# Performance work log

Hardware: AMD Instinct MI355X
Metric: run time of the kernel (lower is better)

The kernel has to match this reference:

```python
import jax, jax.numpy as jnp
import numpy as np
import math

D_MODEL = 1024
EXPAND = 2
D_INNER = D_MODEL * EXPAND          # 2048
D_STATE = 16
NHEADS = 8
NGROUPS = 1
D_CONV = 4
HEADDIM = D_INNER // NHEADS         # 256
CONV_DIM = D_INNER + 2 * NGROUPS * D_STATE   # x, B, C go through the causal conv
D_IN_PROJ = 2 * D_INNER + 2 * NGROUPS * D_STATE + NHEADS  # z, xBC, dt
CHUNK = 64
BATCH = 4
SEQLEN = 4096


def setup_inputs() -> dict:
    key = jax.random.key(0)
    ks = jax.random.split(key, 6)
    rng = np.random.default_rng(0)
    u = jax.random.normal(ks[0], (BATCH, SEQLEN, D_MODEL), dtype=jnp.float32)
    W_in = jax.random.normal(ks[1], (D_MODEL, D_IN_PROJ), dtype=jnp.float32) * 0.02
    conv_w = jax.random.normal(ks[2], (CONV_DIM, D_CONV), dtype=jnp.float32) * (1.0 / math.sqrt(D_CONV))
    conv_b = jnp.zeros((CONV_DIM,), dtype=jnp.float32)
    # dt_bias = inverse-softplus of dt sampled log-uniform in [dt_min, dt_max]
    dt = np.exp(rng.uniform(size=NHEADS) * (math.log(0.1) - math.log(0.001)) + math.log(0.001))
    dt = np.clip(dt, 1e-4, None)
    dt_bias = jnp.asarray(dt + np.log(-np.expm1(-dt)), dtype=jnp.float32)
    # A in A_init_range=(0.9, 0.999), stored as A_log with A = -exp(A_log)
    A_log = jnp.asarray(np.log(rng.uniform(0.9, 0.999, NHEADS)), dtype=jnp.float32)
    D = jnp.ones((NHEADS,), dtype=jnp.float32)
    norm_w = jnp.ones((D_INNER,), dtype=jnp.float32)
    W_out = jax.random.normal(ks[3], (D_INNER, D_MODEL), dtype=jnp.float32) * 0.02
    return {"u": u, "W_in": W_in, "conv_w": conv_w, "conv_b": conv_b,
            "dt_bias": dt_bias, "A_log": A_log, "D": D, "norm_w": norm_w, "W_out": W_out}


def _mamba2_fwd(u, W_in, conv_w, conv_b, dt_bias, A_log, D, norm_w, W_out):
    b, l, _ = u.shape
    h, p, n, g, Q = NHEADS, HEADDIM, D_STATE, NGROUPS, CHUNK
    zxbcdt = u @ W_in                                   # [b,l,2*d_inner+2gn+h]
    z = zxbcdt[..., :D_INNER]
    xBC = zxbcdt[..., D_INNER:D_INNER + CONV_DIM]
    dt = jax.nn.softplus(zxbcdt[..., D_INNER + CONV_DIM:] + dt_bias)  # [b,l,h]
    # causal depthwise conv over time (d_conv taps) + SiLU
    xp = jnp.pad(xBC, ((0, 0), (D_CONV - 1, 0), (0, 0)))
    xconv = conv_b
    for k in range(D_CONV):
        xconv = xconv + xp[:, k:k + l, :] * conv_w[:, k]
    xBC = jax.nn.silu(xconv)
    x = xBC[..., :D_INNER].reshape(b, l, h, p)
    B = xBC[..., D_INNER:D_INNER + g * n].reshape(b, l, g, n)
    C = xBC[..., D_INNER + g * n:].reshape(b, l, g, n)
    Bh = jnp.repeat(B, h // g, axis=2)                  # [b,l,h,n]
    Ch = jnp.repeat(C, h // g, axis=2)
    A = -jnp.exp(A_log)                                 # [h]
    # ---- chunked (SSD) selective scan ----
    nc = l // Q
    xc = x.reshape(b, nc, Q, h, p)
    dtc = dt.reshape(b, nc, Q, h)
    Bc = Bh.reshape(b, nc, Q, h, n)
    Cc = Ch.reshape(b, nc, Q, h, n)
    a = dtc * A                                         # [b,nc,Q,h]
    cs = jnp.cumsum(a, axis=2).transpose(0, 1, 3, 2)    # [b,nc,h,Q]
    mask = jnp.tril(jnp.ones((Q, Q), dtype=bool))
    L = jnp.where(mask, jnp.exp(cs[..., :, None] - cs[..., None, :]), 0.0)  # [b,nc,h,Q,Q]
    xdt = xc * dtc[..., None]                           # x scaled by dt
    Y_diag = jnp.einsum('bcqhn,bcshn,bchqs,bcshp->bcqhp', Cc, Bc, L, xdt)
    decay_states = jnp.exp(cs[..., -1:] - cs)           # [b,nc,h,Q]
    states = jnp.einsum('bcqhn,bchq,bcqhp->bchpn', Bc, decay_states, xdt)  # per-chunk state
    chunk_decay = jnp.exp(cs[..., -1])                  # [b,nc,h]
    def step(carry, inp):
        st, dec = inp
        new = dec[..., None, None] * carry + st
        return new, carry
    init = jnp.zeros((b, h, p, n), dtype=u.dtype)
    _, prev = jax.lax.scan(step, init, (states.transpose(1, 0, 2, 3, 4), chunk_decay.transpose(1, 0, 2)))
    prev = prev.transpose(1, 0, 2, 3, 4)                # state entering each chunk [b,nc,h,p,n]
    Y_off = jnp.einsum('bcqhn,bchpn,bchq->bcqhp', Cc, prev, jnp.exp(cs))
    y = (Y_diag + Y_off).reshape(b, l, h, p) + D[:, None] * x
    y = y.reshape(b, l, D_INNER)
    # gated RMSNorm then out projection
    y = y * jax.nn.silu(z)
    y = y * jax.lax.rsqrt(jnp.mean(y * y, axis=-1, keepdims=True) + 1e-5) * norm_w
    return y @ W_out


def reference(u, W_in, conv_w, conv_b, dt_bias, A_log, D, norm_w, W_out):
    return _mamba2_fwd(u, W_in, conv_w, conv_b, dt_bias, A_log, D, norm_w, W_out)
```

## Files before the change

kernel.cpp:

```cpp
#include <hip/hip_runtime.h>
#include <cstddef>
#include <cstdint>

constexpr int DM = 1024;
constexpr int DI = 2048;
constexpr int DS = 16;
constexpr int NH = 8;
constexpr int CD = 2080;
constexpr int DP = 4136;
constexpr int DPT = 4352;
constexpr int Q  = 64;
constexpr int B_ = 4;
constexpr int L_ = 4096;
constexpr int NCH = 64;
constexpr int HP = 256;
constexpr int NR = B_ * L_;

constexpr size_t AL(size_t x) { return (x + 255) & ~(size_t)255; }
constexpr size_t OFFB_ZX = 0;
constexpr size_t OFFB_BC = AL(OFFB_ZX + (size_t)NR * DP * 2);
constexpr size_t OFFB_DT = AL(OFFB_BC + (size_t)NR * 32 * 4);
constexpr size_t OFFB_CS = AL(OFFB_DT + (size_t)NR * NH * 4);
constexpr size_t OFFB_ST = AL(OFFB_CS + (size_t)B_ * NCH * NH * Q * 4);
constexpr size_t OFFB_Y  = AL(OFFB_ST + (size_t)B_ * NCH * NH * HP * DS * 4);
constexpr size_t OFFB_WO = AL(OFFB_Y + (size_t)NR * DI * 2);

__device__ __forceinline__ float silu_f(float x) { return x / (1.f + expf(-x)); }
__device__ __forceinline__ float bf2f(unsigned short v) {
  unsigned int u = ((unsigned int)v) << 16;
  return __builtin_bit_cast(float, u);
}
__device__ __forceinline__ unsigned short f2bf(float f) {
  unsigned int u = __builtin_bit_cast(unsigned int, f);
  u += 0x7FFFu + ((u >> 16) & 1u);
  return (unsigned short)(u >> 16);
}

typedef __attribute__((ext_vector_type(8))) short bf16x8;
typedef __attribute__((ext_vector_type(4))) float f32x4;

__device__ __forceinline__ void bar() {
  asm volatile("" ::: "memory");
  __builtin_amdgcn_s_barrier();
  asm volatile("" ::: "memory");
}

template<bool OUT_BF16>
__global__ __launch_bounds__(512, 2)
void gemm256(const unsigned short* __restrict__ A, const unsigned short* __restrict__ Bt,
             void* __restrict__ Cout, int M, int N, int K, int ldc) {
  __shared__ __align__(16) unsigned short ring[4][2][256 * 32];
  const int t = threadIdx.x;
  const int w = t >> 6, l = t & 63;
  const int quad = l >> 4, lan = l & 15;
  const int wm = w >> 2, wn = w & 3;
  const int ncol = gridDim.x;
  const int id = blockIdx.y * ncol + blockIdx.x;
  const int xcd = id & 7, slot0 = id >> 3;
  const int rpx = gridDim.y >> 3;
  const int row_g = xcd * rpx + slot0 / ncol;
  const int col_g = slot0 - (slot0 / ncol) * ncol;
  const int row0 = row_g * 256, col0 = col_g * 256;

  const int NSLOT = K >> 5;

  auto stage = [&](int s, int mat) {
    const int ss = (s < NSLOT) ? s : 0;
    const unsigned short* G = mat ? Bt : A;
    const int b0 = mat ? col0 : row0;
    unsigned short* lb = ring[s & 3][mat];
    const int k0 = ss << 5;
    #pragma unroll
    for (int i = 0; i < 2; ++i) {
      const int f = i * 512 + t;
      const int pair = f >> 3, sp = f & 7;
      const int sl = sp ^ (pair & 7);
      const int r = pair * 2 + (sl >> 2);
      const int c16 = sl & 3;
      const unsigned short* gp = G + (size_t)(b0 + r) * K + k0 + (c16 << 3);
      __builtin_amdgcn_global_load_lds(
          (const __attribute__((address_space(1))) void*)gp,
          (__attribute__((address_space(3))) void*)(lb + (size_t)f * 8), 16, 0, 0);
    }
  };

  auto frag = [&](const unsigned short* base, int r, int q) -> bf16x8 {
    const int pair = r >> 1;
    const int sp = (((r & 1) << 2) | q) ^ (pair & 7);
    return *(const bf16x8*)&base[pair * 64 + sp * 8];
  };

  f32x4 acc[2][4][4];
  #pragma unroll
  for (int rq = 0; rq < 2; ++rq)
    #pragma unroll
    for (int mi = 0; mi < 4; ++mi)
      #pragma unroll
      for (int ni = 0; ni < 4; ++ni)
        acc[rq][mi][ni] = (f32x4)(0.0f);

  stage(0, 0); stage(0, 1);
  stage(1, 0); stage(1, 1);
  stage(2, 0); stage(2, 1);

  for (int s = 0; s < NSLOT; ++s) {
    asm volatile("s_waitcnt vmcnt(8)" ::: "memory");
    bar();
    const unsigned short* Aslot = ring[s & 3][0];
    const unsigned short* Bslot = ring[s & 3][1];
    bf16x8 af[4], bf[4];
    #pragma unroll
    for (int ni = 0; ni < 4; ++ni)
      bf[ni] = frag(Bslot, wn * 64 + ni * 16 + lan, quad);
    #pragma unroll
    for (int mi = 0; mi < 4; ++mi)
      af[mi] = frag(Aslot, wm * 128 + mi * 16 + lan, quad);
    stage(s + 3, 0);
    __builtin_amdgcn_s_setprio(1);
    #pragma unroll
    for (int mi = 0; mi < 4; ++mi)
      #pragma unroll
      for (int ni = 0; ni < 4; ++ni)
        acc[0][mi][ni] = __builtin_amdgcn_mfma_f32_16x16x32_bf16(af[mi], bf[ni], acc[0][mi][ni], 0, 0, 0);
    __builtin_amdgcn_s_setprio(0);
    #pragma unroll
    for (int mi = 0; mi < 4; ++mi)
      af[mi] = frag(Aslot, wm * 128 + 64 + mi * 16 + lan, quad);
    stage(s + 3, 1);
    __builtin_amdgcn_s_setprio(1);
    #pragma unroll
    for (int mi = 0; mi < 4; ++mi)
      #pragma unroll
      for (int ni = 0; ni < 4; ++ni)
        acc[1][mi][ni] = __builtin_amdgcn_mfma_f32_16x16x32_bf16(af[mi], bf[ni], acc[1][mi][ni], 0, 0, 0);
    __builtin_amdgcn_s_setprio(0);
    bar();
  }
  asm volatile("s_waitcnt vmcnt(0)" ::: "memory");

  #pragma unroll
  for (int rq = 0; rq < 2; ++rq)
    #pragma unroll
    for (int mi = 0; mi < 4; ++mi) {
      const size_t rb = row0 + wm * 128 + rq * 64 + mi * 16 + quad * 4;
      #pragma unroll
      for (int ni = 0; ni < 4; ++ni) {
        const int colb = col0 + wn * 64 + ni * 16 + lan;
        if (colb < N) {
          if constexpr (OUT_BF16) {
            unsigned short* C = (unsigned short*)Cout;
            #pragma unroll
            for (int r = 0; r < 4; ++r)
              C[(rb + r) * (size_t)ldc + colb] = f2bf(acc[rq][mi][ni][r]);
          } else {
            float* C = (float*)Cout;
            #pragma unroll
            for (int r = 0; r < 4; ++r)
              C[(rb + r) * (size_t)ldc + colb] = acc[rq][mi][ni][r];
          }
        }
      }
    }
}

__global__ __launch_bounds__(256)
void cvt_bf16(const float* __restrict__ src, unsigned short* __restrict__ dst, size_t n4) {
  const size_t i = ((size_t)blockIdx.x * 256 + threadIdx.x) * 4;
  if (i < n4 * 4) {
    float4 v = *(const float4*)(src + i);
    ushort4 o;
    o.x = f2bf(v.x); o.y = f2bf(v.y); o.z = f2bf(v.z); o.w = f2bf(v.w);
    *(ushort4*)(dst + i) = o;
  }
}

__global__ __launch_bounds__(256)
void transpose_cvt(const float* __restrict__ src, unsigned short* __restrict__ dst,
                   int R, int C, int Cvalid) {
  __shared__ float T[64][65];
  const int t = threadIdx.x;
  const int n0 = blockIdx.x * 64, k0 = blockIdx.y * 64;
  #pragma unroll
  for (int i = 0; i < 4; ++i) {
    int f = t + i * 256;
    int r = f >> 4, c4 = (f & 15) << 2;
    int n = n0 + c4;
    float4 v = make_float4(0.f, 0.f, 0.f, 0.f);
    if (n + 3 < Cvalid) {
      v = *(const float4*)(src + (size_t)(k0 + r) * C + n);
    } else {
      if (n + 0 < Cvalid) v.x = src[(size_t)(k0 + r) * C + n + 0];
      if (n + 1 < Cvalid) v.y = src[(size_t)(k0 + r) * C + n + 1];
      if (n + 2 < Cvalid) v.z = src[(size_t)(k0 + r) * C + n + 2];
      if (n + 3 < Cvalid) v.w = src[(size_t)(k0 + r) * C + n + 3];
    }
    T[r][c4 + 0] = v.x; T[r][c4 + 1] = v.y; T[r][c4 + 2] = v.z; T[r][c4 + 3] = v.w;
  }
  __syncthreads();
  #pragma unroll
  for (int i = 0; i < 4; ++i) {
    int f = t + i * 256;
    int c = f >> 4, r4 = (f & 15) << 2;
    ushort4 o;
    o.x = f2bf(T[r4 + 0][c]); o.y = f2bf(T[r4 + 1][c]);
    o.z = f2bf(T[r4 + 2][c]); o.w = f2bf(T[r4 + 3][c]);
    *(ushort4*)(dst + (size_t)(n0 + c) * R + k0 + r4) = o;
  }
}

__global__ __launch_bounds__(256)
void convbc_kernel(const unsigned short* __restrict__ zx, const float* __restrict__ cw,
                   const float* __restrict__ cb, float* __restrict__ bc) {
  const int idx = blockIdx.x * 256 + threadIdx.x;
  const int j = idx & 31;
  const int row = idx >> 5;
  const int l = row & (L_ - 1);
  const int cc = DI + j;
  float a = cb[cc];
  #pragma unroll
  for (int k = 0; k < 4; ++k) {
    int ll = l - 3 + k;
    if (ll >= 0)
      a += bf2f(zx[(size_t)(row - 3 + k) * DP + (DI + DI + j)]) * cw[cc * 4 + k];
  }
  bc[(size_t)row * 32 + j] = silu_f(a);
}

__global__ __launch_bounds__(256)
void dt_kernel(const unsigned short* __restrict__ zx, const float* __restrict__ dt_bias,
               float* __restrict__ dt) {
  const int i = blockIdx.x * 256 + threadIdx.x;
  const int h = i & 7;
  const size_t row = (size_t)(i >> 3);
  float x = bf2f(zx[row * DP + (DI + CD) + h]) + dt_bias[h];
  dt[i] = (x > 20.f) ? x : log1pf(expf(x));
}

__global__ __launch_bounds__(256)
void chunk_kernel(const unsigned short* __restrict__ zx, const float* __restrict__ bc,
                  const float* __restrict__ dt, const float* __restrict__ A_log,
                  const float* __restrict__ cw, const float* __restrict__ cb,
                  const float* __restrict__ Dp, float* __restrict__ cs_out,
                  float* __restrict__ states, unsigned short* __restrict__ yb) {
  const int c = blockIdx.x, h = blockIdx.y, b = blockIdx.z;
  const int t = threadIdx.x;
  const int w = t >> 6, l = t & 63;
  const int quad = l >> 4, lan = l & 15;
  __shared__ float dtS[Q], csS[Q], ddS[Q];
  __shared__ float BsS[Q][DS + 1];
  __shared__ __align__(16) unsigned short Msd[Q][Q + 8];
  __shared__ __align__(16) unsigned short BdT[DS][Q + 8];
  __shared__ __align__(16) char regionA[Q * (Q + 8) * 2];
  __shared__ __align__(16) char regionB[Q * DS * 4 + Q * (Q + 8) * 2];
  float (*CsS)[DS]                 = (float(*)[DS])regionA;
  unsigned short (*xsT)[Q + 8]     = (unsigned short(*)[Q + 8])regionA;
  unsigned short (*rawS)[Q]        = (unsigned short(*)[Q])regionB;
  float (*stS)[DS]                 = (float(*)[DS])regionB;
  unsigned short (*ytS)[Q + 8]     = (unsigned short(*)[Q + 8])(regionB + Q * DS * 4);
  const size_t rowb = (size_t)b * L_ + (size_t)c * Q;

  if (t < Q) {
    float dtv = dt[(rowb + t) * NH + h];
    dtS[t] = dtv;
    float s = dtv * (-expf(A_log[h]));
    #pragma unroll
    for (int off = 1; off < 64; off <<= 1) {
      float n = __shfl_up(s, off, 64);
      if (t >= off) s += n;
    }
    csS[t] = s;
    float slast = __shfl(s, 63, 64);
    ddS[t] = expf(slast - s) * dtv;
    cs_out[(((size_t)b * NCH + c) * NH + h) * Q + t] = s;
  }
  for (int i = t; i < Q * DS; i += 256) {
    int q = i >> 4, n = i & 15;
    BsS[q][n] = bc[(rowb + q) * 32 + n];
    CsS[q][n] = bc[(rowb + q) * 32 + 16 + n];
  }
  __syncthreads();
  for (int i = t; i < DS * Q; i += 256) {
    int n = i & 15, q = i >> 4;
    BdT[n][q] = f2bf(BsS[q][n] * ddS[q]);
  }
  const float Dh = Dp[h];
  for (int i = t; i < Q * Q; i += 256) {
    int q = i >> 6, s = i & 63;
    float v = 0.f;
    if (s <= q) {
      float d = 0.f;
      #pragma unroll
      for (int n = 0; n < DS; ++n) d += CsS[q][n] * BsS[s][n];
      v = expf(csS[q] - csS[s]) * d * dtS[s];
      if (s == q) v += Dh;
    }
    Msd[q][s] = f2bf(v);
  }

  const int pch = l;
  uint4 r0 = make_uint4(0, 0, 0, 0), r1 = make_uint4(0, 0, 0, 0), r2 = make_uint4(0, 0, 0, 0);
  {
    const int col0 = DI + h * HP;
    const unsigned short* gb = zx + ((size_t)b * L_ + (c * Q - 3)) * DP + col0;
    if (c > 0 || t >= 24) r0 = *(const uint4*)(gb + (size_t)(t >> 3) * DP + (t & 7) * 8);
    r1 = *(const uint4*)(gb + (size_t)((t + 256) >> 3) * DP + (t & 7) * 8);
    if (t < 24) r2 = *(const uint4*)(gb + (size_t)((t + 512) >> 3) * DP + (t & 7) * 8);
  }

  for (int pt = 0; pt < 4; ++pt) {
    uint4* rw = (uint4*)rawS;
    rw[t] = r0; rw[t + 256] = r1;
    if (t < 24) rw[t + 512] = r2;
    __syncthreads();
    {
      const int cc = h * HP + pt * Q + pch;
      const float w0 = cw[cc * 4 + 0], w1 = cw[cc * 4 + 1];
      const float w2 = cw[cc * 4 + 2], w3 = cw[cc * 4 + 3];
      const float bias = cb[cc];
      const int q0 = w * 16;
      unsigned short ob[16];
      #pragma unroll
      for (int i2 = 0; i2 < 16; ++i2) {
        int q = q0 + i2;
        float a = bias + bf2f(rawS[q][pch]) * w0 + bf2f(rawS[q + 1][pch]) * w1
                       + bf2f(rawS[q + 2][pch]) * w2 + bf2f(rawS[q + 3][pch]) * w3;
        ob[i2] = f2bf(silu_f(a));
      }
      *(uint4*)&xsT[pch][q0 + 0] = *(uint4*)&ob[0];
      *(uint4*)&xsT[pch][q0 + 8] = *(uint4*)&ob[8];
    }
    if (pt < 3) {
      const int col0n = DI + h * HP + (pt + 1) * Q;
      const unsigned short* gb = zx + ((size_t)b * L_ + (c * Q - 3)) * DP + col0n;
      r0 = make_uint4(0, 0, 0, 0); r2 = make_uint4(0, 0, 0, 0);
      if (c > 0 || t >= 24) r0 = *(const uint4*)(gb + (size_t)(t >> 3) * DP + (t & 7) * 8);
      r1 = *(const uint4*)(gb + (size_t)((t + 256) >> 3) * DP + (t & 7) * 8);
      if (t < 24) r2 = *(const uint4*)(gb + (size_t)((t + 512) >> 3) * DP + (t & 7) * 8);
    }
    __syncthreads();
    bf16x8 xfrag[2];
    #pragma unroll
    for (int ks = 0; ks < 2; ++ks)
      xfrag[ks] = *(const bf16x8*)&xsT[w * 16 + lan][quad * 8 + ks * 32];
    {
      f32x4 sacc = (f32x4)(0.0f);
      #pragma unroll
      for (int ks = 0; ks < 2; ++ks) {
        bf16x8 bfr = *(const bf16x8*)&BdT[lan][quad * 8 + ks * 32];
        sacc = __builtin_amdgcn_mfma_f32_16x16x32_bf16(xfrag[ks], bfr, sacc, 0, 0, 0);
      }
      #pragma unroll
      for (int r = 0; r < 4; ++r)
        stS[w * 16 + quad * 4 + r][lan] = sacc[r];
    }
    {
      #pragma unroll
      for (int mi = 0; mi < 4; ++mi) {
        f32x4 yac = (f32x4)(0.0f);
        #pragma unroll
        for (int ks = 0; ks < 2; ++ks) {
          bf16x8 am = *(const bf16x8*)&Msd[mi * 16 + lan][quad * 8 + ks * 32];
          yac = __builtin_amdgcn_mfma_f32_16x16x32_bf16(am, xfrag[ks], yac, 0, 0, 0);
        }
        #pragma unroll
        for (int r = 0; r < 4; ++r)
          ytS[mi * 16 + quad * 4 + r][w * 16 + lan] = f2bf(yac[r]);
      }
    }
    __syncthreads();
    {
      const size_t stbase = ((((size_t)b * NCH + c) * NH + h) * HP + (size_t)pt * Q) * DS;
      ((float4*)(states + stbase))[t] = ((const float4*)&stS[0][0])[t];
    }
    {
      const int colbase = h * HP + pt * Q;
      #pragma unroll
      for (int pass = 0; pass < 2; ++pass) {
        int q = pass * 32 + (t >> 3), p8 = (t & 7) * 8;
        *(uint4*)(yb + (rowb + q) * (size_t)DI + colbase + p8) = *(const uint4*)&ytS[q][p8];
      }
    }
    __syncthreads();
  }
}

__global__ __launch_bounds__(256)
void scan_kernel(float* __restrict__ states, const float* __restrict__ cs) {
  const int pn = blockIdx.x * 256 + threadIdx.x;
  const int h = blockIdx.y, b = blockIdx.z;
  const size_t cstride = (size_t)NH * HP * DS;
  const size_t base = ((size_t)b * NCH * NH + h) * (size_t)(HP * DS) + pn;
  float carry = 0.f;
  for (int c = 0; c < NCH; ++c) {
    float dec = expf(cs[(((size_t)b * NCH + c) * NH + h) * Q + (Q - 1)]);
    float st = states[base + (size_t)c * cstride];
    states[base + (size_t)c * cstride] = carry;
    carry = dec * carry + st;
  }
}

__global__ __launch_bounds__(256)
void yoff_kernel(const float* __restrict__ bc, const float* __restrict__ cs,
                 const float* __restrict__ prev, unsigned short* __restrict__ yb) {
  const int c = blockIdx.x, h = blockIdx.y, b = blockIdx.z;
  const int t = threadIdx.x;
  __shared__ __align__(16) float CsS[Q][DS];
  __shared__ float ecs[Q];
  const size_t rowb = (size_t)b * L_ + (size_t)c * Q;
  const size_t pb = (((size_t)b * NCH + c) * NH + h) * (size_t)(HP * DS);
  for (int i = t; i < Q * DS; i += 256) {
    int q = i >> 4, n = i & 15;
    CsS[q][n] = bc[(rowb + q) * 32 + 16 + n];
  }
  if (t < Q) ecs[t] = expf(cs[(((size_t)b * NCH + c) * NH + h) * Q + t]);
  float pv[16];
  #pragma unroll
  for (int k = 0; k < 4; ++k)
    *(float4*)&pv[k * 4] = *(const float4*)(prev + pb + (size_t)t * DS + k * 4);
  __syncthreads();
  for (int q = 0; q < Q; ++q) {
    float acc = 0.f;
    #pragma unroll
    for (int n = 0; n < DS; ++n) acc += CsS[q][n] * pv[n];
    const size_t idx = (rowb + q) * DI + h * HP + t;
    yb[idx] = f2bf(bf2f(yb[idx]) + ecs[q] * acc);
  }
}

__global__ __launch_bounds__(256)
void gatenorm_kernel(const unsigned short* __restrict__ zx, const float* __restrict__ norm_w,
                     unsigned short* __restrict__ yb) {
  const size_t row = blockIdx.x;
  const int t = threadIdx.x;
  const unsigned short* zrow = zx + row * DP;
  unsigned short* yrow = yb + row * DI;
  const int d0 = t * 8;
  uint4 yv = *(const uint4*)(yrow + d0);
  uint4 zv = *(const uint4*)(zrow + d0);
  const unsigned short* ys = (const unsigned short*)&yv;
  const unsigned short* zs = (const unsigned short*)&zv;
  float v[8];
  float ss = 0.f;
  #pragma unroll
  for (int j = 0; j < 8; ++j) {
    float val = bf2f(ys[j]) * silu_f(bf2f(zs[j]));
    v[j] = val;
    ss += val * val;
  }
  #pragma unroll
  for (int off = 32; off > 0; off >>= 1) ss += __shfl_down(ss, off);
  __shared__ float red[4];
  if ((t & 63) == 0) red[t >> 6] = ss;
  __syncthreads();
  float tot = red[0] + red[1] + red[2] + red[3];
  float scale = rsqrtf(tot / (float)DI + 1e-5f);
  ushort4 o[2];
  unsigned short* op = (unsigned short*)o;
  #pragma unroll
  for (int j = 0; j < 8; ++j) op[j] = f2bf(v[j] * scale * norm_w[d0 + j]);
  *(uint4*)(yrow + d0) = *(uint4*)o;
}

extern "C" void kernel_launch(void* const* d_in, const int* in_sizes, int n_in,
                              void* d_out, int out_size, void* d_ws, size_t ws_size,
                              hipStream_t stream) {
  const float* u       = (const float*)d_in[0];
  const float* W_in    = (const float*)d_in[1];
  const float* conv_w  = (const float*)d_in[2];
  const float* conv_b  = (const float*)d_in[3];
  const float* dt_bias = (const float*)d_in[4];
  const float* A_log   = (const float*)d_in[5];
  const float* Dp      = (const float*)d_in[6];
  const float* norm_w  = (const float*)d_in[7];
  const float* W_out   = (const float*)d_in[8];
  float* out = (float*)d_out;
  char* w = (char*)d_ws;

  unsigned short* zx  = (unsigned short*)(w + OFFB_ZX);
  float* bcb          = (float*)(w + OFFB_BC);
  float* dtb          = (float*)(w + OFFB_DT);
  float* csb          = (float*)(w + OFFB_CS);
  float* stb          = (float*)(w + OFFB_ST);
  unsigned short* yb  = (unsigned short*)(w + OFFB_Y);
  unsigned short* ub  = (unsigned short*)(w + OFFB_ST);
  unsigned short* wib = (unsigned short*)(w + OFFB_Y);
  unsigned short* wob = (unsigned short*)(w + OFFB_WO);

  cvt_bf16<<<(NR * DM / 4 + 255) / 256, 256, 0, stream>>>(u, ub, (size_t)NR * DM / 4);
  transpose_cvt<<<dim3(DPT / 64, DM / 64), 256, 0, stream>>>(W_in, wib, DM, DP, DP);
  transpose_cvt<<<dim3(DM / 64, DI / 64), 256, 0, stream>>>(W_out, wob, DI, DM, DM);
  gemm256<true><<<dim3(DPT / 256, NR / 256), 512, 0, stream>>>(
      ub, wib, zx, NR, DP, DM, DP);
  convbc_kernel<<<(NR * 32) / 256, 256, 0, stream>>>(zx, conv_w, conv_b, bcb);
  dt_kernel<<<(NR * NH) / 256, 256, 0, stream>>>(zx, dt_bias, dtb);
  chunk_kernel<<<dim3(NCH, NH, B_), 256, 0, stream>>>(zx, bcb, dtb, A_log, conv_w,
                                                      conv_b, Dp, csb, stb, yb);
  scan_kernel<<<dim3((HP * DS) / 256, NH, B_), 256, 0, stream>>>(stb, csb);
  yoff_kernel<<<dim3(NCH, NH, B_), 256, 0, stream>>>(bcb, csb, stb, yb);
  gatenorm_kernel<<<NR, 256, 0, stream>>>(zx, norm_w, yb);
  gemm256<false><<<dim3(DM / 256, NR / 256), 512, 0, stream>>>(
      yb, wob, out, NR, DM, DI, DM);
}
```

Before: 540.2 us.

## Restructure GEMM pipeline to double-buffered 64-wide K tiles with four barrier phases

Replaces the four-slot ring of 32-wide K slices with a two-stage double buffer of 64-wide K tiles, each split into two 32-wide halves. The main loop runs four phases per tile, each issuing one stage load for the next tile and doing one MFMA block between barriers, in a ping-pong style schedule. The aim is to interleave global-to-LDS loads with MFMA work more evenly and to reduce per-iteration waits. It adds more barriers per tile and cuts prefetch depth from three slices ahead to one tile ahead, which may expose memory latency.

```diff
diff --git a/kernel.cpp b/kernel.cpp
--- a/kernel.cpp
+++ b/kernel.cpp
@@ -49,7 +49,7 @@
 __global__ __launch_bounds__(512, 2)
 void gemm256(const unsigned short* __restrict__ A, const unsigned short* __restrict__ Bt,
              void* __restrict__ Cout, int M, int N, int K, int ldc) {
-  __shared__ __align__(16) unsigned short ring[4][2][256 * 32];
+  __shared__ __align__(16) unsigned short lds[2][2][2][256 * 32];
   const int t = threadIdx.x;
   const int w = t >> 6, l = t & 63;
   const int quad = l >> 4, lan = l & 15;
@@ -62,14 +62,14 @@
   const int col_g = slot0 - (slot0 / ncol) * ncol;
   const int row0 = row_g * 256, col0 = col_g * 256;
 
-  const int NSLOT = K >> 5;
-
-  auto stage = [&](int s, int mat) {
-    const int ss = (s < NSLOT) ? s : 0;
+  const int NT = K >> 6;
+
+  auto stage = [&](int tt, int kk, int mat) {
+    const int ss = (tt < NT) ? tt : 0;
     const unsigned short* G = mat ? Bt : A;
     const int b0 = mat ? col0 : row0;
-    unsigned short* lb = ring[s & 3][mat];
-    const int k0 = ss << 5;
+    unsigned short* lb = lds[tt & 1][kk][mat];
+    const int k0 = (ss << 6) + (kk << 5);
     #pragma unroll
     for (int i = 0; i < 2; ++i) {
       const int f = i * 512 + t;
@@ -99,42 +99,41 @@
       for (int ni = 0; ni < 4; ++ni)
         acc[rq][mi][ni] = (f32x4)(0.0f);
 
-  stage(0, 0); stage(0, 1);
-  stage(1, 0); stage(1, 1);
-  stage(2, 0); stage(2, 1);
-
-  for (int s = 0; s < NSLOT; ++s) {
-    asm volatile("s_waitcnt vmcnt(8)" ::: "memory");
-    bar();
-    const unsigned short* Aslot = ring[s & 3][0];
-    const unsigned short* Bslot = ring[s & 3][1];
-    bf16x8 af[4], bf[4];
-    #pragma unroll
-    for (int ni = 0; ni < 4; ++ni)
-      bf[ni] = frag(Bslot, wn * 64 + ni * 16 + lan, quad);
-    #pragma unroll
-    for (int mi = 0; mi < 4; ++mi)
-      af[mi] = frag(Aslot, wm * 128 + mi * 16 + lan, quad);
-    stage(s + 3, 0);
-    __builtin_amdgcn_s_setprio(1);
-    #pragma unroll
-    for (int mi = 0; mi < 4; ++mi)
-      #pragma unroll
-      for (int ni = 0; ni < 4; ++ni)
-        acc[0][mi][ni] = __builtin_amdgcn_mfma_f32_16x16x32_bf16(af[mi], bf[ni], acc[0][mi][ni], 0, 0, 0);
-    __builtin_amdgcn_s_setprio(0);
-    #pragma unroll
-    for (int mi = 0; mi < 4; ++mi)
-      af[mi] = frag(Aslot, wm * 128 + 64 + mi * 16 + lan, quad);
-    stage(s + 3, 1);
-    __builtin_amdgcn_s_setprio(1);
-    #pragma unroll
-    for (int mi = 0; mi < 4; ++mi)
-      #pragma unroll
-      for (int ni = 0; ni < 4; ++ni)
-        acc[1][mi][ni] = __builtin_amdgcn_mfma_f32_16x16x32_bf16(af[mi], bf[ni], acc[1][mi][ni], 0, 0, 0);
-    __builtin_amdgcn_s_setprio(0);
-    bar();
+  stage(0, 0, 0); stage(0, 0, 1);
+  stage(0, 1, 0); stage(0, 1, 1);
+  asm volatile("s_waitcnt vmcnt(4)" ::: "memory");
+  bar();
+
+  for (int tt = 0; tt < NT; ++tt) {
+    const int cur = tt & 1;
+    bf16x8 bf[4];
+    #pragma unroll
+    for (int p = 0; p < 4; ++p) {
+      const int kk = p >> 1, rq = p & 1;
+      const unsigned short* As = lds[cur][kk][0];
+      const unsigned short* Bs = lds[cur][kk][1];
+      bf16x8 af[4];
+      #pragma unroll
+      for (int mi = 0; mi < 4; ++mi)
+        af[mi] = frag(As, wm * 128 + rq * 64 + mi * 16 + lan, quad);
+      if (rq == 0) {
+        #pragma unroll
+        for (int ni = 0; ni < 4; ++ni)
+          bf[ni] = frag(Bs, wn * 64 + ni * 16 + lan, quad);
+      }
+      stage(tt + 1, kk, rq);
+      if (rq == 1)
+        asm volatile("s_waitcnt vmcnt(4)" ::: "memory");
+      bar();
+      __builtin_amdgcn_s_setprio(1);
+      #pragma unroll
+      for (int mi = 0; mi < 4; ++mi)
+        #pragma unroll
+        for (int ni = 0; ni < 4; ++ni)
+          acc[rq][mi][ni] = __builtin_amdgcn_mfma_f32_16x16x32_bf16(af[mi], bf[ni], acc[rq][mi][ni], 0, 0, 0);
+      __builtin_amdgcn_s_setprio(0);
+      bar();
+    }
   }
   asm volatile("s_waitcnt vmcnt(0)" ::: "memory");
 
```

Measured after the change: 532.8 us. About the same (-1.4%).
